# Performance work log

Hardware: AMD Instinct MI355X
Metric: run time of the kernel (lower is better)

Reference implementation:

```python
import jax, jax.numpy as jnp
import numpy as np

B, N, D, D_A, S, D_K = 512, 8192, 1024, 512, 8, 64

def setup_inputs() -> dict:
    key = jax.random.key(0)
    k1, k2, k3, k4 = jax.random.split(key, 4)
    lecun_q = 1.0 / np.sqrt(D_A)
    lecun_k = 1.0 / np.sqrt(D)
    return {
        "z": jax.random.normal(k1, (B, D_A), dtype=jnp.float32),
        "pool_vectors": jax.random.normal(k2, (N, D), dtype=jnp.float32),
        "W_Q": jax.random.normal(k3, (S, D_A, D_K), dtype=jnp.float32) * lecun_q,
        "W_K": jax.random.normal(k4, (S, D, D_K), dtype=jnp.float32) * lecun_k,
        "aspect_logits": jnp.zeros((S,), dtype=jnp.float32),
        "tau": jnp.asarray(0.5, dtype=jnp.float32),
        "lambda_sharp": jnp.asarray(10.0, dtype=jnp.float32),
        "temperature": jnp.asarray(0.1, dtype=jnp.float32),
    }

def reference(z, pool_vectors, W_Q, W_K, aspect_logits, tau, lambda_sharp, temperature):
    # Per-aspect projections
    queries = jnp.einsum('bd,adq->baq', z, W_Q)              # [B, S, d_k]
    keys = jnp.einsum('np,apq->naq', pool_vectors, W_K)       # [N, S, d_k]
    # L2 normalize along d_k
    q_norm = queries / (jnp.linalg.norm(queries, axis=-1, keepdims=True) + 1e-08)
    k_norm = keys / (jnp.linalg.norm(keys, axis=-1, keepdims=True) + 1e-08)
    # Multi-aspect cosine similarity
    sims = jnp.einsum('baq,naq->bna', q_norm, k_norm)          # [B, N, S]
    # Learned aspect weighting
    w = jax.nn.softmax(aspect_logits)                          # [S]
    scores = jnp.einsum('bna,a->bn', sims, w)                  # [B, N]
    # Sigmoid gate against threshold, temperature-scaled normalize
    g = jax.nn.sigmoid(lambda_sharp * (scores - tau))
    alpha_raw = g * jnp.exp(scores / temperature)
    alpha = alpha_raw / (jnp.sum(alpha_raw, axis=-1, keepdims=True) + 1e-08)
    return (alpha, scores, keys)
```

## Files before the change

### kernel.cpp

```cpp
#include <hip/hip_runtime.h>
#include <stdint.h>

#define B_DIM 512
#define N_DIM 8192
#define D_DIM 1024
#define DA_DIM 512
#define S_DIM 8
#define DK_DIM 64
#define C_DIM 512

typedef short v8s __attribute__((ext_vector_type(8)));
typedef float v4f __attribute__((ext_vector_type(4)));

__device__ __forceinline__ unsigned int f2bf(float x) {
    union { float f; unsigned int u; } v; v.f = x;
    unsigned int u = v.u;
    return (u + 0x7fffu + ((u >> 16) & 1u)) >> 16;
}

__device__ __forceinline__ void gld16(const unsigned short* g, unsigned short* l) {
    __builtin_amdgcn_global_load_lds(
        (const __attribute__((address_space(1))) unsigned int*)g,
        (__attribute__((address_space(3))) unsigned int*)l,
        16, 0, 0);
}

__device__ __forceinline__ void cvt8(const float* __restrict__ src,
                                     unsigned short* __restrict__ dst, int t) {
    const float4* s4 = (const float4*)src;
    float4 a = s4[2 * t], b = s4[2 * t + 1];
    uint4 o;
    o.x = f2bf(a.x) | (f2bf(a.y) << 16);
    o.y = f2bf(a.z) | (f2bf(a.w) << 16);
    o.z = f2bf(b.x) | (f2bf(b.y) << 16);
    o.w = f2bf(b.z) | (f2bf(b.w) << 16);
    ((uint4*)dst)[t] = o;
}

__device__ __forceinline__ void w_transpose_tile(const float* __restrict__ w,
                                                 unsigned short* __restrict__ wt,
                                                 int a, int dt, int ddim,
                                                 unsigned short* T ) {
    int t = threadIdx.x;
    int d0 = dt * 64;
    int kc4 = (t & 15) * 4;
    const float4* src = (const float4*)(w + ((size_t)a * ddim + d0) * DK_DIM);
    #pragma unroll
    for (int p = 0; p < 4; p++) {
        int dr = p * 16 + (t >> 4);
        float4 v = src[dr * 16 + (t & 15)];
        uint2 pk;
        pk.x = f2bf(v.x) | (f2bf(v.y) << 16);
        pk.y = f2bf(v.z) | (f2bf(v.w) << 16);
        *(uint2*)&T[dr * 68 + kc4] = pk;
    }
    __syncthreads();
    int c0 = a * 64;
    #pragma unroll
    for (int q = 0; q < 2; q++) {
        int k = q * 32 + (t >> 3);
        int ch = t & 7;
        unsigned short s[8];
        #pragma unroll
        for (int i = 0; i < 8; i++) s[i] = T[(ch * 8 + i) * 68 + k];
        uint4 o;
        o.x = (unsigned)s[0] | ((unsigned)s[1] << 16);
        o.y = (unsigned)s[2] | ((unsigned)s[3] << 16);
        o.z = (unsigned)s[4] | ((unsigned)s[5] << 16);
        o.w = (unsigned)s[6] | ((unsigned)s[7] << 16);
        *(uint4*)&wt[(size_t)(c0 + k) * ddim + d0 + ch * 8] = o;
    }
}

__global__ __launch_bounds__(256) void prep(const float* __restrict__ pool,
                                            const float* __restrict__ z,
                                            const float* __restrict__ W_Q,
                                            const float* __restrict__ W_K,
                                            unsigned short* __restrict__ poolb,
                                            unsigned short* __restrict__ zb,
                                            unsigned short* __restrict__ wqt,
                                            unsigned short* __restrict__ wtb) {
    __shared__ unsigned short T[64 * 68];
    int blk = blockIdx.x;
    if (blk < 4096) {
        cvt8(pool, poolb, blk * 256 + threadIdx.x);
    } else if (blk < 4224) {
        cvt8(z, zb, (blk - 4096) * 256 + threadIdx.x);
    } else if (blk < 4352) {
        int idx = blk - 4224;
        w_transpose_tile(W_K, wtb, idx >> 4, idx & 15, D_DIM, T);
    } else {
        int idx = blk - 4352;
        w_transpose_tile(W_Q, wqt, idx >> 3, idx & 7, DA_DIM, T);
    }
}

__device__ __forceinline__ void gemm_mainloop(const unsigned short* __restrict__ A, int lda,
                                              const unsigned short* __restrict__ Bm, int ldb,
                                              int mbase, int nbase, int kiters,
                                              unsigned short (*As)[4096],
                                              unsigned short (*Bs)[2048],
                                              v4f acc[2][4]) {
    int tid = threadIdx.x;
    int wid = tid >> 6, lane = tid & 63;
    int quad = lane >> 4, l16 = lane & 15;
    int srow = lane >> 2;
    int scol = (lane & 3) * 8;

    auto stage = [&](int kk, int p) {
        #pragma unroll
        for (int j = 0; j < 3; j++) {
            int g = wid * 3 + j;
            if (g < 8) {
                int row = g * 16 + srow;
                gld16(&A[(size_t)(mbase + row) * lda + kk * 32 + scol], &As[p][g * 512]);
            } else {
                int row = (g - 8) * 16 + srow;
                gld16(&Bm[(size_t)(nbase + row) * ldb + kk * 32 + scol], &Bs[p][(g - 8) * 512]);
            }
        }
    };

    stage(0, 0);
    for (int kk = 0; kk < kiters; kk++) {
        __syncthreads();
        if (kk + 1 < kiters) stage(kk + 1, (kk + 1) & 1);
        int p = kk & 1;
        v8s af[2], bf[4];
        #pragma unroll
        for (int mt = 0; mt < 2; mt++)
            af[mt] = *(const v8s*)&As[p][(wid * 32 + mt * 16 + l16) * 32 + quad * 8];
        #pragma unroll
        for (int nt = 0; nt < 4; nt++)
            bf[nt] = *(const v8s*)&Bs[p][(nt * 16 + l16) * 32 + quad * 8];
        #pragma unroll
        for (int mt = 0; mt < 2; mt++)
            #pragma unroll
            for (int nt = 0; nt < 4; nt++)
                acc[mt][nt] = __builtin_amdgcn_mfma_f32_16x16x32_bf16(
                    af[mt], bf[nt], acc[mt][nt], 0, 0, 0);
    }
}

__global__ __launch_bounds__(256, 2) void fused_gemms(const unsigned short* __restrict__ poolb,
                                                      const unsigned short* __restrict__ wtb,
                                                      const unsigned short* __restrict__ zb,
                                                      const unsigned short* __restrict__ wqt,
                                                      const float* __restrict__ logits,
                                                      float* __restrict__ keys_out,
                                                      unsigned short* __restrict__ kb,
                                                      unsigned short* __restrict__ qwb) {
    __shared__ unsigned short As[2][4096];
    __shared__ unsigned short Bs[2][2048];
    v4f acc[2][4];
    #pragma unroll
    for (int mt = 0; mt < 2; mt++)
        #pragma unroll
        for (int nt = 0; nt < 4; nt++) acc[mt][nt] = (v4f)(0.f);

    int blk = blockIdx.x;
    bool is_q = blk >= 512;
    int mbase, nbase;
    if (is_q) {
        int q = blk - 512;
        mbase = (q >> 3) * 128; nbase = (q & 7) * 64;
        gemm_mainloop(zb, DA_DIM, wqt, DA_DIM, mbase, nbase, DA_DIM / 32, As, Bs, acc);
    } else {
        mbase = (blk >> 3) * 128; nbase = (blk & 7) * 64;
        gemm_mainloop(poolb, D_DIM, wtb, D_DIM, mbase, nbase, D_DIM / 32, As, Bs, acc);
    }

    int tid = threadIdx.x, wid = tid >> 6, lane = tid & 63;
    int quad = lane >> 4, l16 = lane & 15;

    if (is_q) {
        float l[8]; float mx = -1e30f;
        #pragma unroll
        for (int i = 0; i < 8; i++) { l[i] = logits[i]; mx = fmaxf(mx, l[i]); }
        float se = 0.f;
        #pragma unroll
        for (int i = 0; i < 8; i++) { l[i] = __expf(l[i] - mx); se += l[i]; }
        float wa = l[nbase >> 6] / se;

        #pragma unroll
        for (int mt = 0; mt < 2; mt++)
            #pragma unroll
            for (int r = 0; r < 4; r++) {
                float ss = 0.f;
                #pragma unroll
                for (int nt = 0; nt < 4; nt++) ss += acc[mt][nt][r] * acc[mt][nt][r];
                ss += __shfl_xor(ss, 1, 64);
                ss += __shfl_xor(ss, 2, 64);
                ss += __shfl_xor(ss, 4, 64);
                ss += __shfl_xor(ss, 8, 64);
                float sc = wa / (sqrtf(ss) + 1e-8f);
                int row = mbase + wid * 32 + mt * 16 + quad * 4 + r;
                #pragma unroll
                for (int nt = 0; nt < 4; nt++) {
                    int col = nbase + nt * 16 + l16;
                    qwb[(size_t)row * C_DIM + col] =
                        (unsigned short)f2bf(acc[mt][nt][r] * sc);
                }
            }
    } else {
        #pragma unroll
        for (int mt = 0; mt < 2; mt++)
            #pragma unroll
            for (int r = 0; r < 4; r++) {
                float ss = 0.f;
                #pragma unroll
                for (int nt = 0; nt < 4; nt++) ss += acc[mt][nt][r] * acc[mt][nt][r];
                ss += __shfl_xor(ss, 1, 64);
                ss += __shfl_xor(ss, 2, 64);
                ss += __shfl_xor(ss, 4, 64);
                ss += __shfl_xor(ss, 8, 64);
                float sc = 1.0f / (sqrtf(ss) + 1e-8f);
                int row = mbase + wid * 32 + mt * 16 + quad * 4 + r;
                #pragma unroll
                for (int nt = 0; nt < 4; nt++) {
                    int col = nbase + nt * 16 + l16;
                    float s = acc[mt][nt][r];
                    keys_out[(size_t)row * C_DIM + col] = s;
                    kb[(size_t)row * C_DIM + col] = (unsigned short)f2bf(s * sc);
                }
            }
    }
}

__global__ __launch_bounds__(256, 2) void scores_gemm(const unsigned short* __restrict__ qwb,
                                                      const unsigned short* __restrict__ kb,
                                                      float* __restrict__ scores_out,
                                                      float* __restrict__ partials,
                                                      const float* __restrict__ lam_p,
                                                      const float* __restrict__ tau_p,
                                                      const float* __restrict__ temp_p) {
    __shared__ unsigned short As[2][4096];
    __shared__ unsigned short Bs[2][2048];
    __shared__ float rowpart[128];
    v4f acc[2][4];
    #pragma unroll
    for (int mt = 0; mt < 2; mt++)
        #pragma unroll
        for (int nt = 0; nt < 4; nt++) acc[mt][nt] = (v4f)(0.f);

    int mbase = blockIdx.y * 128, nbase = blockIdx.x * 64;
    gemm_mainloop(qwb, C_DIM, kb, C_DIM, mbase, nbase, C_DIM / 32, As, Bs, acc);

    int tid = threadIdx.x, wid = tid >> 6, lane = tid & 63;
    int quad = lane >> 4, l16 = lane & 15;

    float lam = lam_p[0], tau = tau_p[0], invT = 1.0f / temp_p[0];

    #pragma unroll
    for (int mt = 0; mt < 2; mt++)
        #pragma unroll
        for (int r = 0; r < 4; r++) {
            float rs = 0.f;
            int row = mbase + wid * 32 + mt * 16 + quad * 4 + r;
            #pragma unroll
            for (int nt = 0; nt < 4; nt++) {
                float s = acc[mt][nt][r];
                int col = nbase + nt * 16 + l16;
                scores_out[(size_t)row * N_DIM + col] = s;
                float g = 1.0f / (1.0f + __expf(-lam * (s - tau)));
                rs += g * __expf(s * invT);
            }
            rs += __shfl_xor(rs, 1, 64);
            rs += __shfl_xor(rs, 2, 64);
            rs += __shfl_xor(rs, 4, 64);
            rs += __shfl_xor(rs, 8, 64);
            if (l16 == 0)
                rowpart[wid * 32 + mt * 16 + quad * 4 + r] = rs;
        }
    __syncthreads();
    if (tid < 128)
        partials[(size_t)blockIdx.x * B_DIM + mbase + tid] = rowpart[tid];
}

__global__ __launch_bounds__(256) void alpha_kernel(const float* __restrict__ scores,
                                                    const float* __restrict__ partials,
                                                    float* __restrict__ alpha,
                                                    const float* __restrict__ lam_p,
                                                    const float* __restrict__ tau_p,
                                                    const float* __restrict__ temp_p) {
    __shared__ float red[128];
    __shared__ float s_inv;
    int b = blockIdx.x;
    int tid = threadIdx.x;
    if (tid < 128) red[tid] = partials[(size_t)tid * B_DIM + b];
    __syncthreads();
    if (tid < 64) {
        float v = red[tid] + red[tid + 64];
        v += __shfl_xor(v, 1, 64);
        v += __shfl_xor(v, 2, 64);
        v += __shfl_xor(v, 4, 64);
        v += __shfl_xor(v, 8, 64);
        v += __shfl_xor(v, 16, 64);
        v += __shfl_xor(v, 32, 64);
        if (tid == 0) s_inv = 1.0f / (v + 1e-8f);
    }
    __syncthreads();
    float inv = s_inv;
    float lam = lam_p[0], tau = tau_p[0], invT = 1.0f / temp_p[0];
    const float4* srow = (const float4*)(scores + (size_t)b * N_DIM);
    float4* arow = (float4*)(alpha + (size_t)b * N_DIM);
    #pragma unroll
    for (int i = 0; i < 8; i++) {
        int idx = tid + i * 256;
        float4 s4 = srow[idx];
        float4 o;
        o.x = (1.0f / (1.0f + __expf(-lam * (s4.x - tau)))) * __expf(s4.x * invT) * inv;
        o.y = (1.0f / (1.0f + __expf(-lam * (s4.y - tau)))) * __expf(s4.y * invT) * inv;
        o.z = (1.0f / (1.0f + __expf(-lam * (s4.z - tau)))) * __expf(s4.z * invT) * inv;
        o.w = (1.0f / (1.0f + __expf(-lam * (s4.w - tau)))) * __expf(s4.w * invT) * inv;
        arow[idx] = o;
    }
}

extern "C" void kernel_launch(void* const* d_in, const int* in_sizes, int n_in,
                              void* d_out, int out_size, void* d_ws, size_t ws_size,
                              hipStream_t stream) {
    const float* z      = (const float*)d_in[0];
    const float* pool   = (const float*)d_in[1];
    const float* W_Q    = (const float*)d_in[2];
    const float* W_K    = (const float*)d_in[3];
    const float* logits = (const float*)d_in[4];
    const float* tau    = (const float*)d_in[5];
    const float* lam    = (const float*)d_in[6];
    const float* temp   = (const float*)d_in[7];

    float* alpha  = (float*)d_out;
    float* scores = alpha + (size_t)B_DIM * N_DIM;
    float* keys   = scores + (size_t)B_DIM * N_DIM;

    char* ws = (char*)d_ws;
    unsigned short* poolb = (unsigned short*)(ws);
    unsigned short* kb    = (unsigned short*)(ws + 16777216);
    unsigned short* wtb   = (unsigned short*)(ws + 25165824);
    unsigned short* wqt   = (unsigned short*)(ws + 26214400);
    unsigned short* zb    = (unsigned short*)(ws + 26738688);
    unsigned short* qwb   = (unsigned short*)(ws + 27262976);
    float* partials       = (float*)(ws + 27787264);

    prep<<<dim3(4416), dim3(256), 0, stream>>>(pool, z, W_Q, W_K,
                                               poolb, zb, wqt, wtb);
    fused_gemms<<<dim3(544), dim3(256), 0, stream>>>(poolb, wtb, zb, wqt, logits,
                                                     keys, kb, qwb);
    scores_gemm<<<dim3(128, 4), dim3(256), 0, stream>>>(qwb, kb, scores, partials,
                                                        lam, tau, temp);
    alpha_kernel<<<dim3(512), dim3(256), 0, stream>>>(scores, partials, alpha,
                                                      lam, tau, temp);
}
```

Measured before the change: 147.5 us.

## Replace LDS double-buffered GEMM mainloop with direct global-to-register prefetch pipeline

Removes the shared-memory staging and per-iteration barriers from all three GEMMs. Each wave now loads its A/B MFMA fragments directly from global memory into registers, with a 4-deep software prefetch and the K loop fully unrolled through a template. This drops LDS traffic and synchronization, but B tiles are re-fetched by every wave and rely on cache, and register usage rises.

```diff
diff --git a/kernel.cpp b/kernel.cpp
--- a/kernel.cpp
+++ b/kernel.cpp
@@ -16,13 +16,6 @@
     union { float f; unsigned int u; } v; v.f = x;
     unsigned int u = v.u;
     return (u + 0x7fffu + ((u >> 16) & 1u)) >> 16;
-}
-
-__device__ __forceinline__ void gld16(const unsigned short* g, unsigned short* l) {
-    __builtin_amdgcn_global_load_lds(
-        (const __attribute__((address_space(1))) unsigned int*)g,
-        (__attribute__((address_space(3))) unsigned int*)l,
-        16, 0, 0);
 }
 
 __device__ __forceinline__ void cvt8(const float* __restrict__ src,
@@ -95,50 +88,49 @@
     }
 }
 
-__device__ __forceinline__ void gemm_mainloop(const unsigned short* __restrict__ A, int lda,
-                                              const unsigned short* __restrict__ Bm, int ldb,
-                                              int mbase, int nbase, int kiters,
-                                              unsigned short (*As)[4096],
-                                              unsigned short (*Bs)[2048],
-                                              v4f acc[2][4]) {
+template <int KITERS>
+__device__ __forceinline__ void gemm_pipe(const unsigned short* __restrict__ A, int lda,
+                                          const unsigned short* __restrict__ Bm, int ldb,
+                                          int mbase, int nbase, v4f acc[2][4]) {
+    constexpr int PF = 4;
     int tid = threadIdx.x;
     int wid = tid >> 6, lane = tid & 63;
     int quad = lane >> 4, l16 = lane & 15;
-    int srow = lane >> 2;
-    int scol = (lane & 3) * 8;
-
-    auto stage = [&](int kk, int p) {
-        #pragma unroll
-        for (int j = 0; j < 3; j++) {
-            int g = wid * 3 + j;
-            if (g < 8) {
-                int row = g * 16 + srow;
-                gld16(&A[(size_t)(mbase + row) * lda + kk * 32 + scol], &As[p][g * 512]);
-            } else {
-                int row = (g - 8) * 16 + srow;
-                gld16(&Bm[(size_t)(nbase + row) * ldb + kk * 32 + scol], &Bs[p][(g - 8) * 512]);
-            }
+    const unsigned short* Ab = A + (size_t)(mbase + wid * 32 + l16) * lda + quad * 8;
+    const unsigned short* Bb = Bm + (size_t)(nbase + l16) * ldb + quad * 8;
+
+    v8s apf[PF][2], bpf[PF][4];
+    #pragma unroll
+    for (int s = 0; s < PF; s++) {
+        #pragma unroll
+        for (int mt = 0; mt < 2; mt++)
+            apf[s][mt] = *(const v8s*)(Ab + (size_t)mt * 16 * lda + s * 32);
+        #pragma unroll
+        for (int nt = 0; nt < 4; nt++)
+            bpf[s][nt] = *(const v8s*)(Bb + (size_t)nt * 16 * ldb + s * 32);
+    }
+    #pragma unroll
+    for (int kk = 0; kk < KITERS; kk++) {
+        const int slot = kk % PF;
+        v8s a0 = apf[slot][0], a1 = apf[slot][1];
+        v8s b0 = bpf[slot][0], b1 = bpf[slot][1];
+        v8s b2 = bpf[slot][2], b3 = bpf[slot][3];
+        if (kk + PF < KITERS) {
+            #pragma unroll
+            for (int mt = 0; mt < 2; mt++)
+                apf[slot][mt] = *(const v8s*)(Ab + (size_t)mt * 16 * lda + (kk + PF) * 32);
+            #pragma unroll
+            for (int nt = 0; nt < 4; nt++)
+                bpf[slot][nt] = *(const v8s*)(Bb + (size_t)nt * 16 * ldb + (kk + PF) * 32);
         }
-    };
-
-    stage(0, 0);
-    for (int kk = 0; kk < kiters; kk++) {
-        __syncthreads();
-        if (kk + 1 < kiters) stage(kk + 1, (kk + 1) & 1);
-        int p = kk & 1;
-        v8s af[2], bf[4];
-        #pragma unroll
-        for (int mt = 0; mt < 2; mt++)
-            af[mt] = *(const v8s*)&As[p][(wid * 32 + mt * 16 + l16) * 32 + quad * 8];
-        #pragma unroll
-        for (int nt = 0; nt < 4; nt++)
-            bf[nt] = *(const v8s*)&Bs[p][(nt * 16 + l16) * 32 + quad * 8];
-        #pragma unroll
-        for (int mt = 0; mt < 2; mt++)
-            #pragma unroll
-            for (int nt = 0; nt < 4; nt++)
-                acc[mt][nt] = __builtin_amdgcn_mfma_f32_16x16x32_bf16(
-                    af[mt], bf[nt], acc[mt][nt], 0, 0, 0);
+        acc[0][0] = __builtin_amdgcn_mfma_f32_16x16x32_bf16(a0, b0, acc[0][0], 0, 0, 0);
+        acc[0][1] = __builtin_amdgcn_mfma_f32_16x16x32_bf16(a0, b1, acc[0][1], 0, 0, 0);
+        acc[0][2] = __builtin_amdgcn_mfma_f32_16x16x32_bf16(a0, b2, acc[0][2], 0, 0, 0);
+        acc[0][3] = __builtin_amdgcn_mfma_f32_16x16x32_bf16(a0, b3, acc[0][3], 0, 0, 0);
+        acc[1][0] = __builtin_amdgcn_mfma_f32_16x16x32_bf16(a1, b0, acc[1][0], 0, 0, 0);
+        acc[1][1] = __builtin_amdgcn_mfma_f32_16x16x32_bf16(a1, b1, acc[1][1], 0, 0, 0);
+        acc[1][2] = __builtin_amdgcn_mfma_f32_16x16x32_bf16(a1, b2, acc[1][2], 0, 0, 0);
+        acc[1][3] = __builtin_amdgcn_mfma_f32_16x16x32_bf16(a1, b3, acc[1][3], 0, 0, 0);
     }
 }
 
@@ -150,8 +142,6 @@
                                                       float* __restrict__ keys_out,
                                                       unsigned short* __restrict__ kb,
                                                       unsigned short* __restrict__ qwb) {
-    __shared__ unsigned short As[2][4096];
-    __shared__ unsigned short Bs[2][2048];
     v4f acc[2][4];
     #pragma unroll
     for (int mt = 0; mt < 2; mt++)
@@ -164,10 +154,10 @@
     if (is_q) {
         int q = blk - 512;
         mbase = (q >> 3) * 128; nbase = (q & 7) * 64;
-        gemm_mainloop(zb, DA_DIM, wqt, DA_DIM, mbase, nbase, DA_DIM / 32, As, Bs, acc);
+        gemm_pipe<DA_DIM / 32>(zb, DA_DIM, wqt, DA_DIM, mbase, nbase, acc);
     } else {
         mbase = (blk >> 3) * 128; nbase = (blk & 7) * 64;
-        gemm_mainloop(poolb, D_DIM, wtb, D_DIM, mbase, nbase, D_DIM / 32, As, Bs, acc);
+        gemm_pipe<D_DIM / 32>(poolb, D_DIM, wtb, D_DIM, mbase, nbase, acc);
     }
 
     int tid = threadIdx.x, wid = tid >> 6, lane = tid & 63;
@@ -234,8 +224,6 @@
                                                       const float* __restrict__ lam_p,
                                                       const float* __restrict__ tau_p,
                                                       const float* __restrict__ temp_p) {
-    __shared__ unsigned short As[2][4096];
-    __shared__ unsigned short Bs[2][2048];
     __shared__ float rowpart[128];
     v4f acc[2][4];
     #pragma unroll
@@ -244,7 +232,7 @@
         for (int nt = 0; nt < 4; nt++) acc[mt][nt] = (v4f)(0.f);
 
     int mbase = blockIdx.y * 128, nbase = blockIdx.x * 64;
-    gemm_mainloop(qwb, C_DIM, kb, C_DIM, mbase, nbase, C_DIM / 32, As, Bs, acc);
+    gemm_pipe<C_DIM / 32>(qwb, C_DIM, kb, C_DIM, mbase, nbase, acc);
 
     int tid = threadIdx.x, wid = tid >> 6, lane = tid & 63;
     int quad = lane >> 4, l16 = lane & 15;
```

After: 195.5 us. 32.5% more time.

## Double K-step per pipeline stage and reorder GEMM block mapping

Applied to the files above, without the earlier changes.

The GEMM mainloop now stages 64 K-elements per double-buffer step as two 32-wide sub-tiles instead of one. This halves the number of __syncthreads barriers and gives each wave more MFMA work between barriers, in exchange for doubling LDS per block (about 48KB). The fused projection GEMM also remaps block indices so consecutive blocks share the same B (weight) tile and walk down M, which should improve L2 reuse of weights. The larger LDS footprint may limit how many blocks fit per CU.

```diff
diff --git a/kernel.cpp b/kernel.cpp
--- a/kernel.cpp
+++ b/kernel.cpp
@@ -97,9 +97,9 @@
 
 __device__ __forceinline__ void gemm_mainloop(const unsigned short* __restrict__ A, int lda,
                                               const unsigned short* __restrict__ Bm, int ldb,
-                                              int mbase, int nbase, int kiters,
-                                              unsigned short (*As)[4096],
-                                              unsigned short (*Bs)[2048],
+                                              int mbase, int nbase, int kiters64,
+                                              unsigned short (*As)[2][4096],
+                                              unsigned short (*Bs)[2][2048],
                                               v4f acc[2][4]) {
     int tid = threadIdx.x;
     int wid = tid >> 6, lane = tid & 63;
@@ -108,37 +108,46 @@
     int scol = (lane & 3) * 8;
 
     auto stage = [&](int kk, int p) {
-        #pragma unroll
-        for (int j = 0; j < 3; j++) {
-            int g = wid * 3 + j;
-            if (g < 8) {
+        int k0 = kk * 64;
+        #pragma unroll
+        for (int j = 0; j < 6; j++) {
+            int i = wid * 6 + j;
+            if (i < 16) {
+                int c = i >> 3, g = i & 7;
                 int row = g * 16 + srow;
-                gld16(&A[(size_t)(mbase + row) * lda + kk * 32 + scol], &As[p][g * 512]);
+                gld16(&A[(size_t)(mbase + row) * lda + k0 + c * 32 + scol],
+                      &As[p][c][g * 512]);
             } else {
-                int row = (g - 8) * 16 + srow;
-                gld16(&Bm[(size_t)(nbase + row) * ldb + kk * 32 + scol], &Bs[p][(g - 8) * 512]);
+                int i2 = i - 16;
+                int c = i2 >> 2, g = i2 & 3;
+                int row = g * 16 + srow;
+                gld16(&Bm[(size_t)(nbase + row) * ldb + k0 + c * 32 + scol],
+                      &Bs[p][c][g * 512]);
             }
         }
     };
 
     stage(0, 0);
-    for (int kk = 0; kk < kiters; kk++) {
+    for (int kk = 0; kk < kiters64; kk++) {
         __syncthreads();
-        if (kk + 1 < kiters) stage(kk + 1, (kk + 1) & 1);
+        if (kk + 1 < kiters64) stage(kk + 1, (kk + 1) & 1);
         int p = kk & 1;
-        v8s af[2], bf[4];
-        #pragma unroll
-        for (int mt = 0; mt < 2; mt++)
-            af[mt] = *(const v8s*)&As[p][(wid * 32 + mt * 16 + l16) * 32 + quad * 8];
-        #pragma unroll
-        for (int nt = 0; nt < 4; nt++)
-            bf[nt] = *(const v8s*)&Bs[p][(nt * 16 + l16) * 32 + quad * 8];
-        #pragma unroll
-        for (int mt = 0; mt < 2; mt++)
+        #pragma unroll
+        for (int c = 0; c < 2; c++) {
+            v8s af[2], bf[4];
+            #pragma unroll
+            for (int mt = 0; mt < 2; mt++)
+                af[mt] = *(const v8s*)&As[p][c][(wid * 32 + mt * 16 + l16) * 32 + quad * 8];
             #pragma unroll
             for (int nt = 0; nt < 4; nt++)
-                acc[mt][nt] = __builtin_amdgcn_mfma_f32_16x16x32_bf16(
-                    af[mt], bf[nt], acc[mt][nt], 0, 0, 0);
+                bf[nt] = *(const v8s*)&Bs[p][c][(nt * 16 + l16) * 32 + quad * 8];
+            #pragma unroll
+            for (int mt = 0; mt < 2; mt++)
+                #pragma unroll
+                for (int nt = 0; nt < 4; nt++)
+                    acc[mt][nt] = __builtin_amdgcn_mfma_f32_16x16x32_bf16(
+                        af[mt], bf[nt], acc[mt][nt], 0, 0, 0);
+        }
     }
 }
 
@@ -150,8 +159,8 @@
                                                       float* __restrict__ keys_out,
                                                       unsigned short* __restrict__ kb,
                                                       unsigned short* __restrict__ qwb) {
-    __shared__ unsigned short As[2][4096];
-    __shared__ unsigned short Bs[2][2048];
+    __shared__ unsigned short As[2][2][4096];
+    __shared__ unsigned short Bs[2][2][2048];
     v4f acc[2][4];
     #pragma unroll
     for (int mt = 0; mt < 2; mt++)
@@ -163,11 +172,11 @@
     int mbase, nbase;
     if (is_q) {
         int q = blk - 512;
-        mbase = (q >> 3) * 128; nbase = (q & 7) * 64;
-        gemm_mainloop(zb, DA_DIM, wqt, DA_DIM, mbase, nbase, DA_DIM / 32, As, Bs, acc);
+        mbase = (q & 3) * 128; nbase = (q >> 2) * 64;
+        gemm_mainloop(zb, DA_DIM, wqt, DA_DIM, mbase, nbase, DA_DIM / 64, As, Bs, acc);
     } else {
-        mbase = (blk >> 3) * 128; nbase = (blk & 7) * 64;
-        gemm_mainloop(poolb, D_DIM, wtb, D_DIM, mbase, nbase, D_DIM / 32, As, Bs, acc);
+        mbase = (blk & 63) * 128; nbase = (blk >> 6) * 64;
+        gemm_mainloop(poolb, D_DIM, wtb, D_DIM, mbase, nbase, D_DIM / 64, As, Bs, acc);
     }
 
     int tid = threadIdx.x, wid = tid >> 6, lane = tid & 63;
@@ -234,8 +243,8 @@
                                                       const float* __restrict__ lam_p,
                                                       const float* __restrict__ tau_p,
                                                       const float* __restrict__ temp_p) {
-    __shared__ unsigned short As[2][4096];
-    __shared__ unsigned short Bs[2][2048];
+    __shared__ unsigned short As[2][2][4096];
+    __shared__ unsigned short Bs[2][2][2048];
     __shared__ float rowpart[128];
     v4f acc[2][4];
     #pragma unroll
@@ -244,7 +253,7 @@
         for (int nt = 0; nt < 4; nt++) acc[mt][nt] = (v4f)(0.f);
 
     int mbase = blockIdx.y * 128, nbase = blockIdx.x * 64;
-    gemm_mainloop(qwb, C_DIM, kb, C_DIM, mbase, nbase, C_DIM / 32, As, Bs, acc);
+    gemm_mainloop(qwb, C_DIM, kb, C_DIM, mbase, nbase, C_DIM / 64, As, Bs, acc);
 
     int tid = threadIdx.x, wid = tid >> 6, lane = tid & 63;
     int quad = lane >> 4, l16 = lane & 15;
```

After: 138.2 us. 1.07x faster.
